# Optimization experiments

Hardware: AMD Instinct MI355X
Metric: run time of the kernel (lower is better)

## Reference

```python
import jax, jax.numpy as jnp
import numpy as np

B, C, H, W = 16, 512, 56, 56
K = 8            # downsample factor
HEADS = 8
EXP = 3          # attn_expansion (int)
HID = HEADS * EXP  # DLA hidden channels = 24
HEAD_DIM = C // HEADS
SCALE = HEAD_DIM ** -0.5
N = H * W
NK = (H // K) * (W // K)
EPS = 1e-5


def conv2d(x, w, stride=1, padding='VALID', groups=1):
    # x: NCHW, w: OIHW
    return jax.lax.conv_general_dilated(
        x, w, (stride, stride), padding,
        dimension_numbers=('NCHW', 'OIHW', 'NCHW'),
        feature_group_count=groups)


def group_norm(x, scale, bias, groups):
    b, c, h, w = x.shape
    xg = x.reshape(b, groups, c // groups, h, w)
    mu = xg.mean(axis=(2, 3, 4), keepdims=True)
    var = xg.var(axis=(2, 3, 4), keepdims=True)
    xg = (xg - mu) * jax.lax.rsqrt(var + EPS)
    x = xg.reshape(b, c, h, w)
    return x * scale[None, :, None, None] + bias[None, :, None, None]


def swish(x):
    return x * jax.nn.sigmoid(x)


def setup_inputs() -> dict:
    key = jax.random.key(0)
    ks = jax.random.split(key, 12)
    s = 0.02
    return {
        'x': jax.random.normal(ks[0], (B, C, H, W), jnp.float32),
        'q_w': jax.random.normal(ks[1], (C, C), jnp.float32) * s,
        'down_w': jax.random.normal(ks[2], (C, 1, K, K), jnp.float32) * s,  # depthwise
        'kv_w': jax.random.normal(ks[3], (C, 2 * C), jnp.float32) * s,
        'proj_w': jax.random.normal(ks[4], (C, C), jnp.float32) * s,
        'proj_b': jnp.zeros((C,), jnp.float32),
        'rel_bias': jax.random.normal(ks[5], (N, NK), jnp.float32) * s,
        'expand_w': jax.random.normal(ks[6], (HID, HEADS, 1, 1), jnp.float32) * s,
        'gn1_s': jnp.ones((HID,), jnp.float32), 'gn1_b': jnp.zeros((HID,), jnp.float32),
        'dw_w': jax.random.normal(ks[7], (HID, 1, 3, 3), jnp.float32) * s,
        'gn2_s': jnp.ones((HID,), jnp.float32), 'gn2_b': jnp.zeros((HID,), jnp.float32),
        'reduce_w': jax.random.normal(ks[8], (HEADS, HID, 1, 1), jnp.float32) * s,
        'gn3_s': jnp.ones((HEADS,), jnp.float32), 'gn3_b': jnp.zeros((HEADS,), jnp.float32),
    }


def dla(a, expand_w, gn1_s, gn1_b, dw_w, gn2_s, gn2_b, reduce_w, gn3_s, gn3_b):
    # a: (B, HEADS, N, NK) treated as NCHW image
    a = swish(group_norm(conv2d(a, expand_w), gn1_s, gn1_b, EXP))
    a = swish(group_norm(conv2d(a, dw_w, padding='SAME', groups=HID), gn2_s, gn2_b, EXP))
    a = group_norm(conv2d(a, reduce_w), gn3_s, gn3_b, 1)
    return a


def reference(x, q_w, down_w, kv_w, proj_w, proj_b, rel_bias,
              expand_w, gn1_s, gn1_b, dw_w, gn2_s, gn2_b,
              reduce_w, gn3_s, gn3_b):
    b = x.shape[0]
    # downsampled kv: depthwise conv kernel=stride=K
    kvx = conv2d(x, down_w, stride=K, groups=C)           # (B, C, H/K, W/K)
    kvx = kvx.reshape(b, C, NK).transpose(0, 2, 1)        # (B, NK, C)
    kv = kvx @ kv_w                                       # (B, NK, 2C)
    kv = kv.reshape(b, NK, 2, HEADS, HEAD_DIM).transpose(2, 0, 3, 1, 4)
    k, v = kv[0], kv[1]                                   # (B, heads, NK, hd)
    q = (x.reshape(b, C, N).transpose(0, 2, 1) @ q_w)     # (B, N, C)
    q = q.reshape(b, N, HEADS, HEAD_DIM).transpose(0, 2, 1, 3)  # (B, heads, N, hd)
    attn = jnp.einsum('bhnd,bhmd->bhnm', q, k) * SCALE + rel_bias
    attn = jax.nn.softmax(attn, axis=-1)
    attn = dla(attn, expand_w, gn1_s, gn1_b, dw_w, gn2_s, gn2_b,
               reduce_w, gn3_s, gn3_b)
    out = jnp.einsum('bhnm,bhmd->bhnd', attn, v)          # (B, heads, N, hd)
    out = out.transpose(0, 2, 1, 3).reshape(b, N, C)      # (B, N, C)
    out = out @ proj_w + proj_b
    # faithful to torch: raw reshape (B, N, C) -> (B, C, H, W), no transpose
    return out.reshape(b, C, H, W)
```

## Files before the change

kernel.cpp:

```cpp
#include <hip/hip_runtime.h>
#include <hip/hip_bf16.h>
#include <stdint.h>

#define B_    16
#define C_    512
#define HIMG  56
#define N_    3136
#define NK_   49
#define NH_   8
#define HD_   64
#define JP_   52
#define J_    416
#define JPQ_  64
#define JQ_   512
#define HID_  24
#define POS_  153664
#define PLH_  9834496
#define CNT_  1229312.0f
#define EPS_  1e-5f
#define SCALE_ 0.125f

typedef __attribute__((ext_vector_type(8))) short short8;
typedef __attribute__((ext_vector_type(4))) float floatx4;

static __device__ __forceinline__ uint16_t f2bf(float f) {
  uint32_t u = __builtin_bit_cast(uint32_t, f);
  u = (u + 0x7FFFu + ((u >> 16) & 1u)) >> 16;
  return (uint16_t)u;
}
static __device__ __forceinline__ float bf2f(uint16_t h) {
  uint32_t u = ((uint32_t)h) << 16;
  return __builtin_bit_cast(float, u);
}
static __device__ __forceinline__ uint16_t f2h(float f) {
  _Float16 h = (_Float16)f;
  return __builtin_bit_cast(uint16_t, h);
}
static __device__ __forceinline__ float h2f(uint16_t u) {
  return (float)__builtin_bit_cast(_Float16, u);
}
static __device__ __forceinline__ float swishf(float z) {
  return z * __builtin_amdgcn_rcpf(1.f + __expf(-z));
}
static __device__ __forceinline__ void ld_attn8(const uint16_t* __restrict__ attn,
                                                size_t off, float* a) {
  uint2 v0 = *(const uint2*)(attn + off);
  uint2 v1 = *(const uint2*)(attn + PLH_ + off);
  a[0] = h2f((uint16_t)(v0.x & 0xFFFFu)); a[1] = h2f((uint16_t)(v0.x >> 16));
  a[2] = h2f((uint16_t)(v0.y & 0xFFFFu)); a[3] = h2f((uint16_t)(v0.y >> 16));
  a[4] = h2f((uint16_t)(v1.x & 0xFFFFu)); a[5] = h2f((uint16_t)(v1.x >> 16));
  a[6] = h2f((uint16_t)(v1.y & 0xFFFFu)); a[7] = h2f((uint16_t)(v1.y >> 16));
}

static __device__ __forceinline__ void gn1_affine(const float* __restrict__ moms,
    const float* __restrict__ ew, const float* __restrict__ gs,
    const float* __restrict__ gb, int b, int g, float* al, float* be) {
  float m1[8];
#pragma unroll
  for (int h = 0; h < 8; ++h) m1[h] = moms[b * 44 + h];
  float sum = 0.f, ssq = 0.f;
#pragma unroll
  for (int o2 = 0; o2 < 8; ++o2) {
    int o = g * 8 + o2;
    float e[8];
#pragma unroll
    for (int h = 0; h < 8; ++h) e[h] = ew[o * 8 + h];
    float so = 0.f;
#pragma unroll
    for (int h = 0; h < 8; ++h) so += e[h] * m1[h];
    sum += so;
    int idx = 8;
#pragma unroll
    for (int h = 0; h < 8; ++h)
#pragma unroll
      for (int h2 = h; h2 < 8; ++h2) {
        float cf = e[h] * e[h2] * ((h == h2) ? 1.f : 2.f);
        ssq += cf * moms[b * 44 + idx];
        ++idx;
      }
  }
  float mean = sum * (1.f / CNT_);
  float var = ssq * (1.f / CNT_) - mean * mean;
  float inv = rsqrtf(var + EPS_);
#pragma unroll
  for (int o2 = 0; o2 < 8; ++o2) {
    al[o2] = inv * gs[g * 8 + o2];
    be[o2] = gb[g * 8 + o2] - mean * al[o2];
  }
}

__global__ __launch_bounds__(256) void k_kvx(const float* __restrict__ x,
                                             const float* __restrict__ dw,
                                             uint16_t* __restrict__ kvxbf,
                                             uint16_t* __restrict__ xbf) {
  int g = blockIdx.x * 256 + threadIdx.x;
  int b = g / (C_ * NK_);
  int rem = g % (C_ * NK_);
  int c = rem / NK_;
  int m = rem % NK_;
  int ph = m / 7, pw = m % 7;
  const size_t base = ((size_t)(b * C_ + c)) * N_ + (ph * 8) * HIMG + pw * 8;
  const float* xp = x + base;
  uint16_t* xbp = xbf + base;
  const float* wp = dw + c * 64;
  float acc = 0.f;
#pragma unroll
  for (int i = 0; i < 8; ++i) {
    float4 a  = *(const float4*)(xp + i * HIMG);
    float4 bq = *(const float4*)(xp + i * HIMG + 4);
    acc += a.x*wp[i*8+0] + a.y*wp[i*8+1] + a.z*wp[i*8+2] + a.w*wp[i*8+3]
         + bq.x*wp[i*8+4] + bq.y*wp[i*8+5] + bq.z*wp[i*8+6] + bq.w*wp[i*8+7];
    uint32_t q0 = (uint32_t)f2bf(a.x)  | ((uint32_t)f2bf(a.y)  << 16);
    uint32_t q1 = (uint32_t)f2bf(a.z)  | ((uint32_t)f2bf(a.w)  << 16);
    uint32_t q2 = (uint32_t)f2bf(bq.x) | ((uint32_t)f2bf(bq.y) << 16);
    uint32_t q3 = (uint32_t)f2bf(bq.z) | ((uint32_t)f2bf(bq.w) << 16);
    *(uint4*)(xbp + (size_t)i * HIMG) = make_uint4(q0, q1, q2, q3);
  }
  kvxbf[((size_t)(b * NK_ + m)) * C_ + c] = f2bf(acc);
}

__global__ __launch_bounds__(256) void k_kv(const uint16_t* __restrict__ kvxbf,
                                            const float* __restrict__ kv_w,
                                            float* __restrict__ kv) {
  const int ct = blockIdx.x, b = blockIdx.y;
  const int j0 = ct * 64;
  const int tid = threadIdx.x, wvid = tid >> 6, lane = tid & 63;
  __shared__ __align__(16) uint32_t A32[64 * 20];
  __shared__ __align__(16) uint32_t B32[64 * 20];
  floatx4 acc[4];
#pragma unroll
  for (int t = 0; t < 4; ++t) acc[t] = (floatx4){0.f,0.f,0.f,0.f};
  const int am = tid & 63, ak = tid >> 6;
  const int bj = tid & 63, bk = tid >> 6;
  for (int ks = 0; ks < 16; ++ks) {
    const int c0 = ks * 32;
    __syncthreads();
    {
      uint4 av = make_uint4(0, 0, 0, 0);
      if (am < NK_)
        av = *(const uint4*)(kvxbf + ((size_t)(b * NK_ + am)) * C_ + c0 + ak * 8);
      *(uint4*)&A32[am * 20 + ak * 4] = av;
    }
    {
      uint32_t pk[4];
#pragma unroll
      for (int r = 0; r < 4; ++r) {
        float f0 = kv_w[(size_t)(c0 + bk * 8 + 2 * r)     * 1024 + j0 + bj];
        float f1 = kv_w[(size_t)(c0 + bk * 8 + 2 * r + 1) * 1024 + j0 + bj];
        pk[r] = (uint32_t)f2bf(f0) | ((uint32_t)f2bf(f1) << 16);
      }
      *(uint4*)&B32[bj * 20 + bk * 4] = make_uint4(pk[0], pk[1], pk[2], pk[3]);
    }
    __syncthreads();
    short8 af = *(const short8*)&A32[(wvid * 16 + (lane & 15)) * 20 + (lane >> 4) * 4];
#pragma unroll
    for (int t = 0; t < 4; ++t) {
      short8 bfb = *(const short8*)&B32[(t * 16 + (lane & 15)) * 20 + (lane >> 4) * 4];
      acc[t] = __builtin_amdgcn_mfma_f32_16x16x32_bf16(af, bfb, acc[t], 0, 0, 0);
    }
  }
  const int rb = wvid * 16 + ((lane >> 4) << 2), cb = lane & 15;
#pragma unroll
  for (int t = 0; t < 4; ++t)
#pragma unroll
    for (int r2 = 0; r2 < 4; ++r2) {
      int m = rb + r2;
      if (m < NK_)
        kv[((size_t)(b * NK_ + m)) * 1024 + j0 + t * 16 + cb] = acc[t][r2];
    }
}

__global__ __launch_bounds__(256) void k_wqk(const float* __restrict__ kv,
                                             const float* __restrict__ q_w,
                                             uint16_t* __restrict__ wqkT) {
  int b = blockIdx.x, h = blockIdx.y;
  __shared__ float ksm[56 * 64];
  for (int idx = threadIdx.x; idx < 56 * 64; idx += 256) {
    int m = idx >> 6, d = idx & 63;
    ksm[idx] = (m < NK_) ? kv[((size_t)(b * NK_ + m)) * 1024 + h * HD_ + d] : 0.f;
  }
  __syncthreads();
#pragma unroll
  for (int cc = 0; cc < 2; ++cc) {
    int c = threadIdx.x + cc * 256;
    float qrow[64];
    const float* qp = q_w + (size_t)c * C_ + h * HD_;
#pragma unroll
    for (int d = 0; d < 64; ++d) qrow[d] = qp[d];
    for (int mc = 0; mc < NK_; mc += 8) {
      int cnt = min(8, NK_ - mc);
      float acc[8] = {0,0,0,0,0,0,0,0};
      for (int d = 0; d < 64; ++d) {
        float q = qrow[d];
#pragma unroll
        for (int i = 0; i < 8; ++i) acc[i] += q * ksm[(mc + i) * 64 + d];
      }
      for (int i = 0; i < cnt; ++i)
        wqkT[((size_t)(b * JQ_ + h * JPQ_ + mc + i)) * C_ + c] = f2bf(acc[i] * SCALE_);
    }
  }
  for (int idx = threadIdx.x; idx < 15 * C_; idx += 256) {
    int rr = idx / C_, c = idx % C_;
    wqkT[((size_t)(b * JQ_ + h * JPQ_ + 49 + rr)) * C_ + c] = 0;
  }
}

__global__ __launch_bounds__(256) void k_wv(const float* __restrict__ kv,
                                            const float* __restrict__ proj_w,
                                            uint16_t* __restrict__ wvT) {
  int b = blockIdx.x, h = blockIdx.y;
  __shared__ float vsm[56 * 64];
  for (int idx = threadIdx.x; idx < 56 * 64; idx += 256) {
    int m = idx >> 6, d = idx & 63;
    vsm[idx] = (m < NK_) ? kv[((size_t)(b * NK_ + m)) * 1024 + 512 + h * HD_ + d] : 0.f;
  }
  __syncthreads();
#pragma unroll
  for (int cc = 0; cc < 2; ++cc) {
    int c = threadIdx.x + cc * 256;
    for (int mc = 0; mc < NK_; mc += 8) {
      int cnt = min(8, NK_ - mc);
      float acc[8] = {0,0,0,0,0,0,0,0};
      for (int d = 0; d < 64; ++d) {
        float w = proj_w[(size_t)(h * HD_ + d) * C_ + c];
#pragma unroll
        for (int i = 0; i < 8; ++i) acc[i] += vsm[(mc + i) * 64 + d] * w;
      }
      uint16_t* dst = wvT + ((size_t)(b * C_ + c)) * J_ + h * JP_ + mc;
      if (cnt == 8) {
        uint32_t pk[4];
#pragma unroll
        for (int i = 0; i < 4; ++i)
          pk[i] = (uint32_t)f2bf(acc[2*i]) | ((uint32_t)f2bf(acc[2*i+1]) << 16);
        *(uint2*)(dst)     = make_uint2(pk[0], pk[1]);
        *(uint2*)(dst + 4) = make_uint2(pk[2], pk[3]);
      } else {
        for (int i = 0; i < cnt; ++i) dst[i] = f2bf(acc[i]);
      }
    }
    uint16_t* pd = wvT + ((size_t)(b * C_ + c)) * J_ + h * JP_ + 49;
    pd[0] = 0; pd[1] = 0; pd[2] = 0;
  }
}

__global__ __launch_bounds__(256) void k_attn(const uint16_t* __restrict__ xbf,
                                              const uint16_t* __restrict__ wqkT,
                                              const float* __restrict__ rel_bias,
                                              uint16_t* __restrict__ attn) {
  const int mt = blockIdx.x, ct = blockIdx.y, b = blockIdx.z;
  const int n0 = mt * 64, jb = ct * 256;
  const int tid = threadIdx.x, wvid = tid >> 6, lane = tid & 63;
  __shared__ __align__(16) char smem[25600 + 64 * 52 * 4];
  uint32_t* A32 = (uint32_t*)smem;
  uint32_t* B32 = (uint32_t*)(smem + 5120);
  uint16_t* eS  = (uint16_t*)smem;
  float* biasS  = (float*)(smem + 25600);

  for (int idx = tid; idx < 64 * NK_; idx += 256) {
    int r = idx / NK_, m = idx - r * NK_;
    biasS[r * 52 + m] = rel_bias[(size_t)(n0 + r) * NK_ + m];
  }

  floatx4 acc[16];
#pragma unroll
  for (int t = 0; t < 16; ++t) acc[t] = (floatx4){0.f,0.f,0.f,0.f};

  const int an = tid & 63, acp = tid >> 6;
  for (int ks = 0; ks < 16; ++ks) {
    const int c0 = ks * 32;
    __syncthreads();
    {
      const uint16_t* xb = xbf + ((size_t)(b * C_ + c0 + acp * 8)) * N_ + n0 + an;
      uint32_t pk[4];
#pragma unroll
      for (int jj = 0; jj < 4; ++jj) {
        uint32_t f0 = xb[(size_t)(2 * jj) * N_];
        uint32_t f1 = xb[(size_t)(2 * jj + 1) * N_];
        pk[jj] = f0 | (f1 << 16);
      }
      *(uint4*)&A32[an * 20 + acp * 4] = make_uint4(pk[0], pk[1], pk[2], pk[3]);
    }
    for (int idx = tid; idx < 1024; idx += 256) {
      int jl = idx >> 2, q = idx & 3;
      uint4 v = *(const uint4*)(wqkT + ((size_t)(b * JQ_ + jb + jl)) * C_ + c0 + q * 8);
      *(uint4*)&B32[jl * 20 + q * 4] = v;
    }
    __syncthreads();
    short8 af = *(const short8*)&A32[(wvid * 16 + (lane & 15)) * 20 + (lane >> 4) * 4];
#pragma unroll
    for (int t = 0; t < 16; ++t) {
      short8 bfb = *(const short8*)&B32[(t * 16 + (lane & 15)) * 20 + (lane >> 4) * 4];
      acc[t] = __builtin_amdgcn_mfma_f32_16x16x32_bf16(af, bfb, acc[t], 0, 0, 0);
    }
  }
  __syncthreads();

  const int rbase = (wvid << 4) + ((lane >> 4) << 2);
  const int cb = lane & 15;
#pragma unroll
  for (int hh = 0; hh < 4; ++hh) {
#pragma unroll
    for (int r2 = 0; r2 < 4; ++r2) {
      const float* bs = &biasS[(rbase + r2) * 52];
      float v0 = acc[hh*4+0][r2] + bs[cb];
      float v1 = acc[hh*4+1][r2] + bs[16 + cb];
      float v2 = acc[hh*4+2][r2] + bs[32 + cb];
      float v3 = (cb == 0) ? (acc[hh*4+3][r2] + bs[48]) : -1e30f;
      float mx = fmaxf(fmaxf(v0, v1), fmaxf(v2, v3));
      mx = fmaxf(mx, __shfl_xor(mx, 1));
      mx = fmaxf(mx, __shfl_xor(mx, 2));
      mx = fmaxf(mx, __shfl_xor(mx, 4));
      mx = fmaxf(mx, __shfl_xor(mx, 8));
      float e0 = __expf(v0 - mx), e1 = __expf(v1 - mx), e2 = __expf(v2 - mx);
      float e3 = (cb == 0) ? __expf(v3 - mx) : 0.f;
      float s = e0 + e1 + e2 + e3;
      s += __shfl_xor(s, 1);
      s += __shfl_xor(s, 2);
      s += __shfl_xor(s, 4);
      s += __shfl_xor(s, 8);
      float inv = __builtin_amdgcn_rcpf(s);
      acc[hh*4+0][r2] = e0 * inv;
      acc[hh*4+1][r2] = e1 * inv;
      acc[hh*4+2][r2] = e2 * inv;
      acc[hh*4+3][r2] = e3 * inv;
    }
  }
#pragma unroll
  for (int hh = 0; hh < 4; ++hh)
#pragma unroll
    for (int tt = 0; tt < 4; ++tt) {
      int m = tt * 16 + cb;
      if (m < NK_) {
#pragma unroll
        for (int r2 = 0; r2 < 4; ++r2)
          eS[((rbase + r2) * NK_ + m) * 4 + hh] = f2h(acc[hh*4+tt][r2]);
      }
    }
  __syncthreads();
  uint16_t* dst = attn + (size_t)ct * PLH_ + ((size_t)b * N_ + n0) * NK_ * 4;
  for (int idx = tid; idx < 64 * NK_; idx += 256)
    *(uint2*)(dst + idx * 4) = *(const uint2*)&eS[idx * 4];
}

__global__ __launch_bounds__(256) void k_moms(const uint16_t* __restrict__ attn,
                                              float* __restrict__ moms) {
  int nt = blockIdx.x, b = blockIdx.y;
  float vals[44];
#pragma unroll
  for (int k = 0; k < 44; ++k) vals[k] = 0.f;
  for (int task = threadIdx.x; task < 64 * NK_; task += 256) {
    float a[8];
    ld_attn8(attn, ((size_t)b * N_ + nt * 64) * NK_ * 4 + (size_t)task * 4, a);
#pragma unroll
    for (int h = 0; h < 8; ++h) vals[h] += a[h];
    int idx = 8;
#pragma unroll
    for (int h = 0; h < 8; ++h)
#pragma unroll
      for (int h2 = h; h2 < 8; ++h2) { vals[idx] += a[h] * a[h2]; ++idx; }
  }
  __shared__ float red[4][44];
  int lane = threadIdx.x & 63, wvid = threadIdx.x >> 6;
#pragma unroll
  for (int k = 0; k < 44; ++k) {
#pragma unroll
    for (int off = 32; off; off >>= 1) vals[k] += __shfl_down(vals[k], off, 64);
  }
  if (lane == 0) {
#pragma unroll
    for (int k = 0; k < 44; ++k) red[wvid][k] = vals[k];
  }
  __syncthreads();
  if (threadIdx.x < 44) {
    float t = red[0][threadIdx.x] + red[1][threadIdx.x] + red[2][threadIdx.x] + red[3][threadIdx.x];
    atomicAdd(&moms[b * 44 + threadIdx.x], t);
  }
}

__global__ void k_aff(const float* __restrict__ moms, const float* __restrict__ ew,
                      const float* __restrict__ gn1_s, const float* __restrict__ gn1_b,
                      float* __restrict__ gn1ab) {
  int t = threadIdx.x;
  if (t >= 48) return;
  int b = t / 3, g = t % 3;
  float al[8], be[8];
  gn1_affine(moms, ew, gn1_s, gn1_b, b, g, al, be);
#pragma unroll
  for (int o = 0; o < 8; ++o) { gn1ab[t * 16 + o] = al[o]; gn1ab[t * 16 + 8 + o] = be[o]; }
}

__global__ void k_aff2(const float* __restrict__ gn2sums, const float* __restrict__ gn2_s,
                       const float* __restrict__ gn2_b, float* __restrict__ gn2ab) {
  int t = threadIdx.x;
  if (t >= 48) return;
  int b = t / 3, g = t % 3;
  float s2 = gn2sums[b * 6 + g * 2], q2 = gn2sums[b * 6 + g * 2 + 1];
  float mean = s2 * (1.f / CNT_);
  float var = q2 * (1.f / CNT_) - mean * mean;
  float inv = rsqrtf(var + EPS_);
#pragma unroll
  for (int o = 0; o < 8; ++o) {
    float al = inv * gn2_s[g * 8 + o];
    gn2ab[t * 16 + o] = al;
    gn2ab[t * 16 + 8 + o] = gn2_b[g * 8 + o] - mean * al;
  }
}

template<bool STORE>
__global__ __launch_bounds__(256) void k_dla0_t(const uint16_t* __restrict__ attn,
    const float* __restrict__ ew, const float* __restrict__ gn1ab,
    const float* __restrict__ dww, float* __restrict__ gn2sums,
    uint16_t* __restrict__ a2buf) {
  const int nt = blockIdx.x, b = blockIdx.y, g = blockIdx.z;
  const int n0 = nt * 16;
  __shared__ __align__(16) float h1s[18 * 51 * 8];
  __shared__ float red[4][2];
  float al[8], be[8];
  {
    const float* ab = gn1ab + (b * 3 + g) * 16;
#pragma unroll
    for (int o = 0; o < 8; ++o) { al[o] = ab[o]; be[o] = ab[8 + o]; }
  }
  for (int task = threadIdx.x; task < 18 * NK_; task += 256) {
    int r = task / NK_, m = task % NK_;
    int n = n0 - 1 + r;
    float h1v[8];
    if (n < 0 || n >= N_) {
#pragma unroll
      for (int o = 0; o < 8; ++o) h1v[o] = 0.f;
    } else {
      float a[8];
      ld_attn8(attn, (((size_t)b * N_ + n) * NK_ + m) * 4, a);
#pragma unroll
      for (int o = 0; o < 8; ++o) {
        float v = 0.f;
#pragma unroll
        for (int h = 0; h < 8; ++h) v += ew[(g * 8 + o) * 8 + h] * a[h];
        h1v[o] = swishf(v * al[o] + be[o]);
      }
    }
    float* dst = &h1s[(r * 51 + m + 1) * 8];
    *(float4*)dst = make_float4(h1v[0], h1v[1], h1v[2], h1v[3]);
    *(float4*)(dst + 4) = make_float4(h1v[4], h1v[5], h1v[6], h1v[7]);
  }
  for (int idx = threadIdx.x; idx < 18 * 16; idx += 256) {
    int r = idx >> 4, c = idx & 15;
    h1s[(r * 51 + (c >> 3) * 50) * 8 + (c & 7)] = 0.f;
  }
  __syncthreads();
  const int row = threadIdx.x >> 4, mg = threadIdx.x & 15;
  const int m0 = mg * 3;
  const int mlim = (mg == 15) ? 4 : 3;
  float a2[4][8];
#pragma unroll
  for (int mi = 0; mi < 4; ++mi)
#pragma unroll
    for (int o = 0; o < 8; ++o) a2[mi][o] = 0.f;
#pragma unroll
  for (int dr = 0; dr < 3; ++dr) {
    float win[48];
    const float* src = &h1s[((row + dr) * 51 + m0) * 8];
#pragma unroll
    for (int k = 0; k < 12; ++k)
      *(float4*)&win[k * 4] = *(const float4*)(src + k * 4);
#pragma unroll
    for (int o = 0; o < 8; ++o) {
      float wa = dww[(g * 8 + o) * 9 + dr * 3 + 0];
      float wb = dww[(g * 8 + o) * 9 + dr * 3 + 1];
      float wc = dww[(g * 8 + o) * 9 + dr * 3 + 2];
#pragma unroll
      for (int mi = 0; mi < 4; ++mi)
        a2[mi][o] += win[mi * 8 + o] * wa + win[(mi + 1) * 8 + o] * wb + win[(mi + 2) * 8 + o] * wc;
    }
  }
  float s0 = 0.f, q0 = 0.f;
#pragma unroll
  for (int mi = 0; mi < 4; ++mi) {
    if (mi < mlim) {
#pragma unroll
      for (int o = 0; o < 8; ++o) { s0 += a2[mi][o]; q0 += a2[mi][o] * a2[mi][o]; }
    }
  }
  int lane = threadIdx.x & 63, wvid = threadIdx.x >> 6;
#pragma unroll
  for (int off = 32; off; off >>= 1) { s0 += __shfl_down(s0, off, 64); q0 += __shfl_down(q0, off, 64); }
  if (lane == 0) { red[wvid][0] = s0; red[wvid][1] = q0; }
  __syncthreads();
  if (threadIdx.x < 2) {
    float t = red[0][threadIdx.x] + red[1][threadIdx.x] + red[2][threadIdx.x] + red[3][threadIdx.x];
    atomicAdd(&gn2sums[b * 6 + g * 2 + threadIdx.x], t);
  }
  if (STORE) {
    uint32_t* a2s = (uint32_t*)h1s;
#pragma unroll
    for (int mi = 0; mi < 4; ++mi) {
      if (mi < mlim) {
        uint32_t pk[4];
#pragma unroll
        for (int q = 0; q < 4; ++q)
          pk[q] = (uint32_t)f2h(a2[mi][2*q]) | ((uint32_t)f2h(a2[mi][2*q+1]) << 16);
        *(uint4*)&a2s[(row * NK_ + m0 + mi) * 4] = make_uint4(pk[0], pk[1], pk[2], pk[3]);
      }
    }
    __syncthreads();
    uint16_t* dstb = a2buf + ((size_t)(b * 3 + g) * POS_ + (size_t)n0 * NK_) * 8;
    for (int idx = threadIdx.x; idx < 16 * NK_; idx += 256)
      *(uint4*)(dstb + (size_t)idx * 8) = *(const uint4*)&a2s[idx * 4];
  }
}

__global__ __launch_bounds__(256) void k_dla1b(const uint16_t* __restrict__ a2buf,
    const float* __restrict__ gn2ab, const float* __restrict__ rww,
    float* __restrict__ gn3sums, uint16_t* __restrict__ rbuf) {
  const int b = blockIdx.y;
  const int pos = blockIdx.x * 256 + threadIdx.x;
  __shared__ float rws[192];
  __shared__ float red[4][2];
  for (int i = threadIdx.x; i < 192; i += 256) rws[i] = rww[i];
  __syncthreads();
  float r[8] = {0.f,0.f,0.f,0.f,0.f,0.f,0.f,0.f};
  if (pos < POS_) {
#pragma unroll
    for (int g = 0; g < 3; ++g) {
      const float* ab = gn2ab + (b * 3 + g) * 16;
      uint4 v = *(const uint4*)(a2buf + ((size_t)(b * 3 + g) * POS_ + pos) * 8);
      uint32_t w[4] = {v.x, v.y, v.z, v.w};
#pragma unroll
      for (int q = 0; q < 4; ++q) {
#pragma unroll
        for (int hl = 0; hl < 2; ++hl) {
          int o = q * 2 + hl;
          float f = h2f((uint16_t)(hl ? (w[q] >> 16) : (w[q] & 0xFFFFu)));
          float sw = swishf(f * ab[o] + ab[8 + o]);
#pragma unroll
          for (int p = 0; p < 8; ++p) r[p] += rws[p * HID_ + g * 8 + o] * sw;
        }
      }
    }
  }
  float sr = 0.f, qr = 0.f;
#pragma unroll
  for (int p = 0; p < 8; ++p) { sr += r[p]; qr += r[p] * r[p]; }
  int lane = threadIdx.x & 63, wvid = threadIdx.x >> 6;
#pragma unroll
  for (int off = 32; off; off >>= 1) { sr += __shfl_down(sr, off, 64); qr += __shfl_down(qr, off, 64); }
  if (lane == 0) { red[wvid][0] = sr; red[wvid][1] = qr; }
  __syncthreads();
  if (threadIdx.x < 2) {
    float t = red[0][threadIdx.x] + red[1][threadIdx.x] + red[2][threadIdx.x] + red[3][threadIdx.x];
    atomicAdd(&gn3sums[b * 2 + threadIdx.x], t);
  }
  if (pos < POS_) {
    int n = pos / NK_, m = pos - n * NK_;
    uint16_t* dst = rbuf + ((size_t)b * N_ + n) * J_;
#pragma unroll
    for (int p = 0; p < 8; ++p) dst[p * JP_ + m] = f2bf(r[p]);
    if (m < 3) {
#pragma unroll
      for (int p = 0; p < 8; ++p) dst[p * JP_ + 49 + m] = 0;
    }
  }
}

__global__ __launch_bounds__(256) void k_dla1s(const uint16_t* __restrict__ attn,
    const float* __restrict__ ew, const float* __restrict__ gn1ab,
    const float* __restrict__ dww, const float* __restrict__ gn2ab,
    const float* __restrict__ rww, float* __restrict__ gn3sums,
    uint16_t* __restrict__ rbuf) {
  const int nt = blockIdx.x, b = blockIdx.y;
  const int n0 = nt * 16;
  __shared__ __align__(16) float h1s[18 * 51 * 8];
  __shared__ float red[4][2];
  const int row = threadIdx.x >> 4, mg = threadIdx.x & 15;
  const int m0 = mg * 3;
  const int mlim = (mg == 15) ? 4 : 3;
  float racc[4][8];
#pragma unroll
  for (int mi = 0; mi < 4; ++mi)
#pragma unroll
    for (int p = 0; p < 8; ++p) racc[mi][p] = 0.f;

  for (int g = 0; g < 3; ++g) {
    float al[8], be[8], al2[8], be2[8];
    {
      const float* ab1 = gn1ab + (b * 3 + g) * 16;
      const float* ab2 = gn2ab + (b * 3 + g) * 16;
#pragma unroll
      for (int o = 0; o < 8; ++o) {
        al[o] = ab1[o]; be[o] = ab1[8 + o];
        al2[o] = ab2[o]; be2[o] = ab2[8 + o];
      }
    }
    __syncthreads();
    for (int task = threadIdx.x; task < 18 * NK_; task += 256) {
      int r = task / NK_, m = task % NK_;
      int n = n0 - 1 + r;
      float h1v[8];
      if (n < 0 || n >= N_) {
#pragma unroll
        for (int o = 0; o < 8; ++o) h1v[o] = 0.f;
      } else {
        float a[8];
        ld_attn8(attn, (((size_t)b * N_ + n) * NK_ + m) * 4, a);
#pragma unroll
        for (int o = 0; o < 8; ++o) {
          float v = 0.f;
#pragma unroll
          for (int h = 0; h < 8; ++h) v += ew[(g * 8 + o) * 8 + h] * a[h];
          h1v[o] = swishf(v * al[o] + be[o]);
        }
      }
      float* dst = &h1s[(r * 51 + m + 1) * 8];
      *(float4*)dst = make_float4(h1v[0], h1v[1], h1v[2], h1v[3]);
      *(float4*)(dst + 4) = make_float4(h1v[4], h1v[5], h1v[6], h1v[7]);
    }
    for (int idx = threadIdx.x; idx < 18 * 16; idx += 256) {
      int r = idx >> 4, c = idx & 15;
      h1s[(r * 51 + (c >> 3) * 50) * 8 + (c & 7)] = 0.f;
    }
    __syncthreads();
    float a2[4][8];
#pragma unroll
    for (int mi = 0; mi < 4; ++mi)
#pragma unroll
      for (int o = 0; o < 8; ++o) a2[mi][o] = 0.f;
#pragma unroll
    for (int dr = 0; dr < 3; ++dr) {
      float win[48];
      const float* src = &h1s[((row + dr) * 51 + m0) * 8];
#pragma unroll
      for (int k = 0; k < 12; ++k)
        *(float4*)&win[k * 4] = *(const float4*)(src + k * 4);
#pragma unroll
      for (int o = 0; o < 8; ++o) {
        float wa = dww[(g * 8 + o) * 9 + dr * 3 + 0];
        float wb = dww[(g * 8 + o) * 9 + dr * 3 + 1];
        float wc = dww[(g * 8 + o) * 9 + dr * 3 + 2];
#pragma unroll
        for (int mi = 0; mi < 4; ++mi)
          a2[mi][o] += win[mi * 8 + o] * wa + win[(mi + 1) * 8 + o] * wb + win[(mi + 2) * 8 + o] * wc;
      }
    }
#pragma unroll
    for (int mi = 0; mi < 4; ++mi) {
      if (mi < mlim) {
#pragma unroll
        for (int o = 0; o < 8; ++o) {
          float sw = swishf(a2[mi][o] * al2[o] + be2[o]);
#pragma unroll
          for (int p = 0; p < 8; ++p) racc[mi][p] += rww[p * HID_ + g * 8 + o] * sw;
        }
      }
    }
  }
  float sr = 0.f, qr = 0.f;
  const int n = n0 + row;
  uint16_t* dstbase = rbuf + ((size_t)b * N_ + n) * J_;
#pragma unroll
  for (int mi = 0; mi < 4; ++mi) {
    if (mi < mlim) {
      int m = m0 + mi;
#pragma unroll
      for (int p = 0; p < 8; ++p) {
        float v = racc[mi][p];
        dstbase[p * JP_ + m] = f2bf(v);
        sr += v; qr += v * v;
      }
    }
  }
  if (mg == 15) {
#pragma unroll
    for (int p = 0; p < 8; ++p) {
      dstbase[p * JP_ + 49] = 0; dstbase[p * JP_ + 50] = 0; dstbase[p * JP_ + 51] = 0;
    }
  }
  int lane = threadIdx.x & 63, wvid = threadIdx.x >> 6;
#pragma unroll
  for (int off = 32; off; off >>= 1) { sr += __shfl_down(sr, off, 64); qr += __shfl_down(qr, off, 64); }
  if (lane == 0) { red[wvid][0] = sr; red[wvid][1] = qr; }
  __syncthreads();
  if (threadIdx.x < 2) {
    float t = red[0][threadIdx.x] + red[1][threadIdx.x] + red[2][threadIdx.x] + red[3][threadIdx.x];
    atomicAdd(&gn3sums[b * 2 + threadIdx.x], t);
  }
}

__global__ __launch_bounds__(256) void k_out(const uint16_t* __restrict__ rr,
    const uint16_t* __restrict__ wvT, const float* __restrict__ gn3sums,
    const float* __restrict__ gn3_s, const float* __restrict__ gn3_b,
    const float* __restrict__ proj_b, float* __restrict__ outp) {
  const int mt = blockIdx.x, ct = blockIdx.y, b = blockIdx.z;
  const int n0 = mt * 64, c0 = ct * 128;
  const int tid = threadIdx.x, wvid = tid >> 6, lane = tid & 63;
  __shared__ __align__(16) uint32_t A32[64 * 20];
  __shared__ __align__(16) uint32_t B32[128 * 20];
  __shared__ float ab3[J_ * 2];
  {
    float ssum = gn3sums[b*2], sq = gn3sums[b*2+1];
    float mean = ssum * (1.f / CNT_);
    float var = sq * (1.f / CNT_) - mean * mean;
    float inv = rsqrtf(var + EPS_);
    for (int j = tid; j < J_; j += 256) {
      int h = j / JP_;
      float al = inv * gn3_s[h];
      ab3[j*2] = al; ab3[j*2+1] = gn3_b[h] - mean * al;
    }
  }
  floatx4 acc[8];
#pragma unroll
  for (int t = 0; t < 8; ++t) acc[t] = (floatx4){0.f,0.f,0.f,0.f};
  const int an = tid >> 2, acp = tid & 3;
  for (int ks = 0; ks < 13; ++ks) {
    const int k0 = ks * 32;
    __syncthreads();
    {
      const uint16_t* src = rr + ((size_t)b * N_ + n0 + an) * J_ + k0 + acp * 8;
      uint4 v = *(const uint4*)src;
      uint32_t raw[4] = {v.x, v.y, v.z, v.w};
      uint32_t pk[4];
#pragma unroll
      for (int jj = 0; jj < 4; ++jj) {
        int j = k0 + acp * 8 + jj * 2;
        float f0 = bf2f((uint16_t)(raw[jj] & 0xFFFFu)) * ab3[j*2]     + ab3[j*2+1];
        float f1 = bf2f((uint16_t)(raw[jj] >> 16))     * ab3[(j+1)*2] + ab3[(j+1)*2+1];
        pk[jj] = (uint32_t)f2bf(f0) | ((uint32_t)f2bf(f1) << 16);
      }
      *(uint4*)&A32[an * 20 + acp * 4] = make_uint4(pk[0], pk[1], pk[2], pk[3]);
    }
    for (int idx = tid; idx < 128 * 4; idx += 256) {
      int rw2 = idx >> 2, q = idx & 3;
      uint4 v = *(const uint4*)(wvT + ((size_t)b * C_ + c0 + rw2) * J_ + k0 + q * 8);
      *(uint4*)&B32[rw2 * 20 + q * 4] = v;
    }
    __syncthreads();
    short8 af = *(const short8*)&A32[(wvid * 16 + (lane & 15)) * 20 + (lane >> 4) * 4];
#pragma unroll
    for (int t = 0; t < 8; ++t) {
      short8 bfb = *(const short8*)&B32[(t * 16 + (lane & 15)) * 20 + (lane >> 4) * 4];
      acc[t] = __builtin_amdgcn_mfma_f32_16x16x32_bf16(af, bfb, acc[t], 0, 0, 0);
    }
  }
  const int rb = wvid * 16 + ((lane >> 4) << 2);
#pragma unroll
  for (int t = 0; t < 8; ++t) {
    int c = c0 + t * 16 + (lane & 15);
    float pb = proj_b[c];
#pragma unroll
    for (int r2 = 0; r2 < 4; ++r2)
      outp[((size_t)b * N_ + n0 + rb + r2) * C_ + c] = acc[t][r2] + pb;
  }
}

extern "C" void kernel_launch(void* const* d_in, const int* in_sizes, int n_in,
                              void* d_out, int out_size, void* d_ws, size_t ws_size,
                              hipStream_t stream) {
  (void)in_sizes; (void)n_in; (void)out_size;
  const float* x      = (const float*)d_in[0];
  const float* q_w    = (const float*)d_in[1];
  const float* down_w = (const float*)d_in[2];
  const float* kv_w   = (const float*)d_in[3];
  const float* proj_w = (const float*)d_in[4];
  const float* proj_b = (const float*)d_in[5];
  const float* rel_b  = (const float*)d_in[6];
  const float* ew     = (const float*)d_in[7];
  const float* gn1_s  = (const float*)d_in[8];
  const float* gn1_b  = (const float*)d_in[9];
  const float* dw_w   = (const float*)d_in[10];
  const float* gn2_s  = (const float*)d_in[11];
  const float* gn2_b  = (const float*)d_in[12];
  const float* red_w  = (const float*)d_in[13];
  const float* gn3_s  = (const float*)d_in[14];
  const float* gn3_b  = (const float*)d_in[15];
  float* outp = (float*)d_out;

  const size_t NEED_SMALL = 109946880;
  const size_t NEED_BIG   = 205924352;
  if (ws_size < NEED_SMALL) return;
  const bool big = (ws_size >= NEED_BIG);

  char* ws = (char*)d_ws;
  uint16_t* xbf   = (uint16_t*)(ws);
  uint16_t* kvxbf = (uint16_t*)(ws + 51380224);
  float*    kv    = (float*)(ws + 52183040);
  uint16_t* wqkT  = (uint16_t*)(ws + 55394304);
  uint16_t* a2    = (uint16_t*)(ws);
  uint16_t* attn;
  uint16_t* wvT;
  uint16_t* rbuf;
  float*    stats;
  if (big) {
    attn  = (uint16_t*)(ws + 118013952);
    wvT   = (uint16_t*)(ws + 157351936);
    rbuf  = (uint16_t*)(ws + 164167680);
    stats = (float*)(ws + 205914112);
  } else {
    wvT   = (uint16_t*)(ws + 63782912);
    attn  = (uint16_t*)(ws + 70598656);
    rbuf  = (uint16_t*)(ws);
    stats = (float*)(ws + 109936640);
  }
  float* moms    = stats;
  float* gn2sums = stats + 704;
  float* gn3sums = stats + 800;
  float* gn1ab   = stats + 1024;
  float* gn2ab   = stats + 1792;

  hipMemsetAsync(stats, 0, 4096, stream);
  k_kvx<<<1568, 256, 0, stream>>>(x, down_w, kvxbf, xbf);
  k_kv<<<dim3(16, 16), 256, 0, stream>>>(kvxbf, kv_w, kv);
  k_wqk<<<dim3(16, 8), 256, 0, stream>>>(kv, q_w, wqkT);
  k_wv<<<dim3(16, 8), 256, 0, stream>>>(kv, proj_w, wvT);
  k_attn<<<dim3(49, 2, 16), 256, 0, stream>>>(xbf, wqkT, rel_b, attn);
  k_moms<<<dim3(49, 16), 256, 0, stream>>>(attn, moms);
  k_aff<<<1, 64, 0, stream>>>(moms, ew, gn1_s, gn1_b, gn1ab);
  if (big) {
    k_dla0_t<true><<<dim3(196, 16, 3), 256, 0, stream>>>(attn, ew, gn1ab, dw_w,
                                                         gn2sums, a2);
    k_aff2<<<1, 64, 0, stream>>>(gn2sums, gn2_s, gn2_b, gn2ab);
    k_dla1b<<<dim3(601, 16), 256, 0, stream>>>(a2, gn2ab, red_w, gn3sums, rbuf);
  } else {
    k_dla0_t<false><<<dim3(196, 16, 3), 256, 0, stream>>>(attn, ew, gn1ab, dw_w,
                                                          gn2sums, nullptr);
    k_aff2<<<1, 64, 0, stream>>>(gn2sums, gn2_s, gn2_b, gn2ab);
    k_dla1s<<<dim3(196, 16), 256, 0, stream>>>(attn, ew, gn1ab, dw_w, gn2ab,
                                               red_w, gn3sums, rbuf);
  }
  k_out<<<dim3(49, 4, 16), 256, 0, stream>>>(rbuf, wvT, gn3sums, gn3_s, gn3_b, proj_b, outp);
}
```

Before: 805.0 us.

## Fuse GN1 moment reduction into attention kernel and interleave all heads

The attention kernel now computes all 8 heads per block instead of splitting them across two planes, and writes attn as 8 interleaved fp16 heads per position with a single 16-byte store. The GN1 moment accumulation that lived in a separate k_moms kernel is now done from registers right after softmax, so the full attn tensor no longer has to be re-read. Downstream loaders use one uint4 load instead of two strided uint2 loads. In exchange the accumulator count doubles to 32 floatx4 plus 44 moment registers, which raises register pressure and halves the grid, possibly lowering occupancy.

```diff
diff --git a/kernel.cpp b/kernel.cpp
--- a/kernel.cpp
+++ b/kernel.cpp
@@ -15,7 +15,6 @@
 #define JQ_   512
 #define HID_  24
 #define POS_  153664
-#define PLH_  9834496
 #define CNT_  1229312.0f
 #define EPS_  1e-5f
 #define SCALE_ 0.125f
@@ -44,12 +43,11 @@
 }
 static __device__ __forceinline__ void ld_attn8(const uint16_t* __restrict__ attn,
                                                 size_t off, float* a) {
-  uint2 v0 = *(const uint2*)(attn + off);
-  uint2 v1 = *(const uint2*)(attn + PLH_ + off);
-  a[0] = h2f((uint16_t)(v0.x & 0xFFFFu)); a[1] = h2f((uint16_t)(v0.x >> 16));
-  a[2] = h2f((uint16_t)(v0.y & 0xFFFFu)); a[3] = h2f((uint16_t)(v0.y >> 16));
-  a[4] = h2f((uint16_t)(v1.x & 0xFFFFu)); a[5] = h2f((uint16_t)(v1.x >> 16));
-  a[6] = h2f((uint16_t)(v1.y & 0xFFFFu)); a[7] = h2f((uint16_t)(v1.y >> 16));
+  uint4 v = *(const uint4*)(attn + off);
+  a[0] = h2f((uint16_t)(v.x & 0xFFFFu)); a[1] = h2f((uint16_t)(v.x >> 16));
+  a[2] = h2f((uint16_t)(v.y & 0xFFFFu)); a[3] = h2f((uint16_t)(v.y >> 16));
+  a[4] = h2f((uint16_t)(v.z & 0xFFFFu)); a[5] = h2f((uint16_t)(v.z >> 16));
+  a[6] = h2f((uint16_t)(v.w & 0xFFFFu)); a[7] = h2f((uint16_t)(v.w >> 16));
 }
 
 static __device__ __forceinline__ void gn1_affine(const float* __restrict__ moms,
@@ -246,24 +244,25 @@
 __global__ __launch_bounds__(256) void k_attn(const uint16_t* __restrict__ xbf,
                                               const uint16_t* __restrict__ wqkT,
                                               const float* __restrict__ rel_bias,
-                                              uint16_t* __restrict__ attn) {
-  const int mt = blockIdx.x, ct = blockIdx.y, b = blockIdx.z;
-  const int n0 = mt * 64, jb = ct * 256;
+                                              uint16_t* __restrict__ attn,
+                                              float* __restrict__ moms) {
+  const int mt = blockIdx.x, b = blockIdx.y;
+  const int n0 = mt * 64;
   const int tid = threadIdx.x, wvid = tid >> 6, lane = tid & 63;
-  __shared__ __align__(16) char smem[25600 + 64 * 52 * 4];
+  __shared__ __align__(16) char smem[60096];
   uint32_t* A32 = (uint32_t*)smem;
   uint32_t* B32 = (uint32_t*)(smem + 5120);
-  uint16_t* eS  = (uint16_t*)smem;
-  float* biasS  = (float*)(smem + 25600);
+  float* biasS  = (float*)(smem + 46080);
+  float (*red)[44] = (float(*)[44])(smem + 59392);
 
   for (int idx = tid; idx < 64 * NK_; idx += 256) {
     int r = idx / NK_, m = idx - r * NK_;
     biasS[r * 52 + m] = rel_bias[(size_t)(n0 + r) * NK_ + m];
   }
 
-  floatx4 acc[16];
-#pragma unroll
-  for (int t = 0; t < 16; ++t) acc[t] = (floatx4){0.f,0.f,0.f,0.f};
+  floatx4 acc[32];
+#pragma unroll
+  for (int t = 0; t < 32; ++t) acc[t] = (floatx4){0.f,0.f,0.f,0.f};
 
   const int an = tid & 63, acp = tid >> 6;
   for (int ks = 0; ks < 16; ++ks) {
@@ -280,25 +279,24 @@
       }
       *(uint4*)&A32[an * 20 + acp * 4] = make_uint4(pk[0], pk[1], pk[2], pk[3]);
     }
-    for (int idx = tid; idx < 1024; idx += 256) {
+    for (int idx = tid; idx < 2048; idx += 256) {
       int jl = idx >> 2, q = idx & 3;
-      uint4 v = *(const uint4*)(wqkT + ((size_t)(b * JQ_ + jb + jl)) * C_ + c0 + q * 8);
+      uint4 v = *(const uint4*)(wqkT + ((size_t)(b * JQ_ + jl)) * C_ + c0 + q * 8);
       *(uint4*)&B32[jl * 20 + q * 4] = v;
     }
     __syncthreads();
     short8 af = *(const short8*)&A32[(wvid * 16 + (lane & 15)) * 20 + (lane >> 4) * 4];
 #pragma unroll
-    for (int t = 0; t < 16; ++t) {
+    for (int t = 0; t < 32; ++t) {
       short8 bfb = *(const short8*)&B32[(t * 16 + (lane & 15)) * 20 + (lane >> 4) * 4];
       acc[t] = __builtin_amdgcn_mfma_f32_16x16x32_bf16(af, bfb, acc[t], 0, 0, 0);
     }
   }
-  __syncthreads();
 
   const int rbase = (wvid << 4) + ((lane >> 4) << 2);
   const int cb = lane & 15;
 #pragma unroll
-  for (int hh = 0; hh < 4; ++hh) {
+  for (int hh = 0; hh < 8; ++hh) {
 #pragma unroll
     for (int r2 = 0; r2 < 4; ++r2) {
       const float* bs = &biasS[(rbase + r2) * 52];
@@ -325,55 +323,50 @@
       acc[hh*4+3][r2] = e3 * inv;
     }
   }
-#pragma unroll
-  for (int hh = 0; hh < 4; ++hh)
-#pragma unroll
-    for (int tt = 0; tt < 4; ++tt) {
-      int m = tt * 16 + cb;
-      if (m < NK_) {
-#pragma unroll
-        for (int r2 = 0; r2 < 4; ++r2)
-          eS[((rbase + r2) * NK_ + m) * 4 + hh] = f2h(acc[hh*4+tt][r2]);
-      }
-    }
+
+  uint16_t* dst = attn + ((size_t)b * N_ + n0) * NK_ * 8;
+  float vals[44];
+#pragma unroll
+  for (int k = 0; k < 44; ++k) vals[k] = 0.f;
+#pragma unroll
+  for (int tt = 0; tt < 4; ++tt) {
+    int m = tt * 16 + cb;
+    if (m < NK_) {
+#pragma unroll
+      for (int r2 = 0; r2 < 4; ++r2) {
+        int row = rbase + r2;
+        float a[8];
+#pragma unroll
+        for (int hh = 0; hh < 8; ++hh) a[hh] = acc[hh*4+tt][r2];
+        uint32_t pk[4];
+#pragma unroll
+        for (int q = 0; q < 4; ++q)
+          pk[q] = (uint32_t)f2h(a[2*q]) | ((uint32_t)f2h(a[2*q+1]) << 16);
+        *(uint4*)(dst + ((size_t)row * NK_ + m) * 8) =
+            make_uint4(pk[0], pk[1], pk[2], pk[3]);
+#pragma unroll
+        for (int h = 0; h < 8; ++h) vals[h] += a[h];
+        int idx = 8;
+#pragma unroll
+        for (int h = 0; h < 8; ++h)
+#pragma unroll
+          for (int h2 = h; h2 < 8; ++h2) { vals[idx] += a[h] * a[h2]; ++idx; }
+      }
+    }
+  }
+#pragma unroll
+  for (int k = 0; k < 44; ++k) {
+#pragma unroll
+    for (int off = 32; off; off >>= 1) vals[k] += __shfl_down(vals[k], off, 64);
+  }
+  if (lane == 0) {
+#pragma unroll
+    for (int k = 0; k < 44; ++k) red[wvid][k] = vals[k];
+  }
   __syncthreads();
-  uint16_t* dst = attn + (size_t)ct * PLH_ + ((size_t)b * N_ + n0) * NK_ * 4;
-  for (int idx = tid; idx < 64 * NK_; idx += 256)
-    *(uint2*)(dst + idx * 4) = *(const uint2*)&eS[idx * 4];
-}
-
-__global__ __launch_bounds__(256) void k_moms(const uint16_t* __restrict__ attn,
-                                              float* __restrict__ moms) {
-  int nt = blockIdx.x, b = blockIdx.y;
-  float vals[44];
-#pragma unroll
-  for (int k = 0; k < 44; ++k) vals[k] = 0.f;
-  for (int task = threadIdx.x; task < 64 * NK_; task += 256) {
-    float a[8];
-    ld_attn8(attn, ((size_t)b * N_ + nt * 64) * NK_ * 4 + (size_t)task * 4, a);
-#pragma unroll
-    for (int h = 0; h < 8; ++h) vals[h] += a[h];
-    int idx = 8;
-#pragma unroll
-    for (int h = 0; h < 8; ++h)
-#pragma unroll
-      for (int h2 = h; h2 < 8; ++h2) { vals[idx] += a[h] * a[h2]; ++idx; }
-  }
-  __shared__ float red[4][44];
-  int lane = threadIdx.x & 63, wvid = threadIdx.x >> 6;
-#pragma unroll
-  for (int k = 0; k < 44; ++k) {
-#pragma unroll
-    for (int off = 32; off; off >>= 1) vals[k] += __shfl_down(vals[k], off, 64);
-  }
-  if (lane == 0) {
-#pragma unroll
-    for (int k = 0; k < 44; ++k) red[wvid][k] = vals[k];
-  }
-  __syncthreads();
-  if (threadIdx.x < 44) {
-    float t = red[0][threadIdx.x] + red[1][threadIdx.x] + red[2][threadIdx.x] + red[3][threadIdx.x];
-    atomicAdd(&moms[b * 44 + threadIdx.x], t);
+  if (tid < 44) {
+    float t = red[0][tid] + red[1][tid] + red[2][tid] + red[3][tid];
+    atomicAdd(&moms[b * 44 + tid], t);
   }
 }
 
@@ -430,7 +423,7 @@
       for (int o = 0; o < 8; ++o) h1v[o] = 0.f;
     } else {
       float a[8];
-      ld_attn8(attn, (((size_t)b * N_ + n) * NK_ + m) * 4, a);
+      ld_attn8(attn, (((size_t)b * N_ + n) * NK_ + m) * 8, a);
 #pragma unroll
       for (int o = 0; o < 8; ++o) {
         float v = 0.f;
@@ -601,7 +594,7 @@
         for (int o = 0; o < 8; ++o) h1v[o] = 0.f;
       } else {
         float a[8];
-        ld_attn8(attn, (((size_t)b * N_ + n) * NK_ + m) * 4, a);
+        ld_attn8(attn, (((size_t)b * N_ + n) * NK_ + m) * 8, a);
 #pragma unroll
         for (int o = 0; o < 8; ++o) {
           float v = 0.f;
@@ -810,8 +803,7 @@
   k_kv<<<dim3(16, 16), 256, 0, stream>>>(kvxbf, kv_w, kv);
   k_wqk<<<dim3(16, 8), 256, 0, stream>>>(kv, q_w, wqkT);
   k_wv<<<dim3(16, 8), 256, 0, stream>>>(kv, proj_w, wvT);
-  k_attn<<<dim3(49, 2, 16), 256, 0, stream>>>(xbf, wqkT, rel_b, attn);
-  k_moms<<<dim3(49, 16), 256, 0, stream>>>(attn, moms);
+  k_attn<<<dim3(49, 16), 256, 0, stream>>>(xbf, wqkT, rel_b, attn, moms);
   k_aff<<<1, 64, 0, stream>>>(moms, ew, gn1_s, gn1_b, gn1ab);
   if (big) {
     k_dla0_t<true><<<dim3(196, 16, 3), 256, 0, stream>>>(attn, ew, gn1ab, dw_w,
```

Result: slower. 860.0 us (+6.8%).
